# Kernel optimization log

Measured on AMD Instinct MI355X. Metric: run time of the kernel, lower is better.

## Reference

```python
import jax, jax.numpy as jnp
import numpy as np

B, T, D = 2, 2048, 1024
HEADS, UNITS = 16, 64
OUT_DIM = 1024
_LARGE_BIAS = 10000.0


def _uniform(key, shape, fan_in, fan_out):
    limit = np.sqrt(6.0 / (fan_in + fan_out))
    return jax.random.uniform(key, shape, jnp.float32, -limit, limit)


def setup_inputs() -> dict:
    key = jax.random.key(0)
    kx, kq, kk, kv, ko = jax.random.split(key, 5)
    x = jax.random.normal(kx, (B, T, D), jnp.float32)
    mask = jnp.ones((B, T), jnp.int32)
    Wq = _uniform(kq, (D, HEADS * UNITS), D, UNITS)
    Wk = _uniform(kk, (D, HEADS * UNITS), D, UNITS)
    Wv = _uniform(kv, (D, HEADS * UNITS), D, UNITS)
    Wo = _uniform(ko, (HEADS * UNITS, OUT_DIM), HEADS * UNITS, OUT_DIM)
    return {"x": x, "mask": mask, "Wq": Wq, "Wk": Wk, "Wv": Wv, "Wo": Wo}


def reference(x, mask, Wq, Wk, Wv, Wo):
    m = mask.astype(x.dtype)                      # [B, T]
    x = x * m[:, :, None]                         # zero padded positions
    b, t, _ = x.shape
    # projections, split heads: [B, T, H, U]
    q = (x @ Wq).reshape(b, t, HEADS, UNITS)
    k = (x @ Wk).reshape(b, t, HEADS, UNITS)
    v = (x @ Wv).reshape(b, t, HEADS, UNITS)
    # logits[b,h,i,j] = sum_u q[b,i,h,u] k[b,j,h,u]
    logits = jnp.einsum('bihu,bjhu->bhij', q, k) / np.sqrt(UNITS).astype(x.dtype)
    # causal (forward) mask: subtract large bias above the diagonal
    causal = jnp.triu(jnp.full((t, t), _LARGE_BIAS, x.dtype), k=1)
    logits = logits - causal
    # padding mask on key axis
    logits = logits - ((1.0 - m) * _LARGE_BIAS)[:, None, None, :]
    weights = jax.nn.softmax(logits, axis=-1)     # [B, H, T, T]
    attended = jnp.einsum('bhij,bjhu->bihu', weights, v)
    attended = attended.reshape(b, t, HEADS * UNITS)
    return attended @ Wo                          # [B, T, OUT_DIM]
```

## Files before the change

kernel.cpp:

```cpp
#include <hip/hip_runtime.h>
#include <stdint.h>
#include <stddef.h>

#define B_ 2
#define T_ 2048
#define D_ 1024
#define H_ 16
#define U_ 64
#define M_ (B_ * T_)
#define N_ (H_ * U_)

typedef __attribute__((ext_vector_type(4))) float f32x4;
typedef __attribute__((ext_vector_type(8))) short s16x8;
typedef __attribute__((ext_vector_type(8))) __bf16 b16x8;

static_assert(sizeof(s16x8) == 16, "frag size");

__device__ __forceinline__ unsigned short f2bf(float f) {
  unsigned int u = __float_as_uint(f);
  u += 0x7FFFu + ((u >> 16) & 1u);
  return (unsigned short)(u >> 16);
}

__device__ __forceinline__ float exp2_hw(float x) {
  float r;
  asm("v_exp_f32 %0, %1" : "=v"(r) : "v"(x));
  return r;
}
__device__ __forceinline__ unsigned int cvtpk_bf16(float lo, float hi) {
  unsigned int r;
  asm("v_cvt_pk_bf16_f32 %0, %1, %2" : "=v"(r) : "v"(lo), "v"(hi));
  return r;
}

template <typename V>
__device__ __forceinline__ auto mfma16_impl(V a, V b, f32x4 c, int)
    -> decltype(__builtin_amdgcn_mfma_f32_16x16x32_bf16(a, b, c, 0, 0, 0)) {
  return __builtin_amdgcn_mfma_f32_16x16x32_bf16(a, b, c, 0, 0, 0);
}
template <typename V>
__device__ __forceinline__ f32x4 mfma16_impl(V a, V b, f32x4 c, long) {
  return __builtin_amdgcn_mfma_f32_16x16x32_bf16(
      __builtin_bit_cast(b16x8, a), __builtin_bit_cast(b16x8, b), c, 0, 0, 0);
}
__device__ __forceinline__ f32x4 mfma16(s16x8 a, s16x8 b, f32x4 c) {
  return mfma16_impl(a, b, c, 0);
}

__device__ __forceinline__ void gld16(const unsigned short* g, unsigned short* l) {
  __builtin_amdgcn_global_load_lds(
      (const __attribute__((address_space(1))) void*)g,
      (__attribute__((address_space(3))) void*)l, 16, 0, 0);
}

__global__ void prep_kernel(const float* __restrict__ x, const int* __restrict__ mask,
                            const float* __restrict__ w0, const float* __restrict__ w1,
                            const float* __restrict__ w2, const float* __restrict__ w3,
                            unsigned short* __restrict__ o0, unsigned short* __restrict__ o1,
                            unsigned short* __restrict__ o2, unsigned short* __restrict__ o3,
                            unsigned short* __restrict__ xb) {
  const int tid = threadIdx.x;
  if (blockIdx.x < 1024) {
    __shared__ float tile[64][65];
    const int id = blockIdx.x;
    const int mz = id >> 8, by = (id >> 4) & 15, bx = id & 15;
    const float* w;
    unsigned short* o;
    switch (mz) {
      case 0: w = w0; o = o0; break;
      case 1: w = w1; o = o1; break;
      case 2: w = w2; o = o2; break;
      default: w = w3; o = o3; break;
    }
    const int kb = by * 64, nb = bx * 64;
    const int r0 = tid >> 6, c = tid & 63;
#pragma unroll
    for (int i = 0; i < 16; i++) {
      int r = i * 4 + r0;
      tile[r][c] = w[(size_t)(kb + r) * 1024 + nb + c];
    }
    __syncthreads();
#pragma unroll
    for (int i = 0; i < 16; i++) {
      int r = i * 4 + r0;
      o[(size_t)(nb + r) * 1024 + kb + c] = f2bf(tile[c][r]);
    }
  } else {
    const int idx = ((blockIdx.x - 1024) * 256 + tid) * 4;
    const int row = idx >> 10;
    const float m = (float)mask[row];
    float4 v = *(const float4*)(x + idx);
    ushort4 o;
    o.x = f2bf(v.x * m);
    o.y = f2bf(v.y * m);
    o.z = f2bf(v.z * m);
    o.w = f2bf(v.w * m);
    *(ushort4*)(xb + idx) = o;
  }
}

template <int MODE>
__device__ __forceinline__ void gemm64_body(const unsigned short* __restrict__ A,
                                            const unsigned short* __restrict__ Bt,
                                            void* __restrict__ Cout) {
  constexpr int Kd = 1024, Nd = 1024;
  __shared__ unsigned short la[128 * 64];
  __shared__ unsigned short lb[128 * 64];
  const int tid = threadIdx.x;
  const int lane = tid & 63;
  const int w = tid >> 6;
  const int mb = blockIdx.y * 128, nb = blockIdx.x * 128;
  const int wm = (w >> 1) * 64, wn = (w & 1) * 64;
  const int lr = lane & 15, lg = lane >> 4;
  const int srow = tid >> 3;
  const int scol = (tid & 7) * 8;
  const int sc = scol ^ ((srow & 7) << 3);
  const unsigned short* gA = A + (size_t)(mb + srow) * Kd + sc;
  const unsigned short* gB = Bt + (size_t)(nb + srow) * Kd + sc;
  unsigned short* lA = la + srow * 64 + scol;
  unsigned short* lB = lb + srow * 64 + scol;
  const int rsw = (lr & 7) << 3;

  f32x4 acc[4][4] = {};

  for (int kt = 0; kt < Kd; kt += 64) {
#pragma unroll
    for (int i = 0; i < 4; i++) {
      gld16(gA + kt + (size_t)(i * 32) * Kd, lA + i * 32 * 64);
      gld16(gB + kt + (size_t)(i * 32) * Kd, lB + i * 32 * 64);
    }
    __syncthreads();
#pragma unroll
    for (int ks = 0; ks < 2; ks++) {
      const int kc = (ks * 32 + lg * 8) ^ rsw;
      s16x8 af[4], bfr[4];
#pragma unroll
      for (int i = 0; i < 4; i++)
        af[i] = *(const s16x8*)(la + (wm + i * 16 + lr) * 64 + kc);
#pragma unroll
      for (int j = 0; j < 4; j++)
        bfr[j] = *(const s16x8*)(lb + (wn + j * 16 + lr) * 64 + kc);
#pragma unroll
      for (int i = 0; i < 4; i++)
#pragma unroll
        for (int j = 0; j < 4; j++)
          acc[i][j] = mfma16(af[i], bfr[j], acc[i][j]);
    }
    __syncthreads();
  }

#pragma unroll
  for (int i = 0; i < 4; i++)
#pragma unroll
    for (int j = 0; j < 4; j++) {
      const int col = nb + wn + j * 16 + lr;
      const int rowb = mb + wm + i * 16 + lg * 4;
      if (MODE == 1) {
        float* C = (float*)Cout;
#pragma unroll
        for (int r = 0; r < 4; r++) C[(size_t)(rowb + r) * Nd + col] = acc[i][j][r];
      } else if (MODE == 0) {
        unsigned short* C = (unsigned short*)Cout;
#pragma unroll
        for (int r = 0; r < 4; r++) C[(size_t)(rowb + r) * Nd + col] = f2bf(acc[i][j][r]);
      } else {
        unsigned short* C = (unsigned short*)Cout;
        const size_t vrow = ((size_t)(rowb >> 11) * 16 + (col >> 6)) * 64 + (col & 63);
        ushort4 o;
#pragma unroll
        for (int r = 0; r < 4; r++) ((unsigned short*)&o)[r] = f2bf(acc[i][j][r]);
        *(ushort4*)(C + vrow * T_ + (rowb & 2047)) = o;
      }
    }
}

__global__ __launch_bounds__(256) void gemm_qkv(const unsigned short* __restrict__ A,
                                                const unsigned short* __restrict__ wq,
                                                const unsigned short* __restrict__ wk,
                                                const unsigned short* __restrict__ wv,
                                                unsigned short* __restrict__ cq,
                                                unsigned short* __restrict__ ck,
                                                unsigned short* __restrict__ vt) {
  if (blockIdx.z == 0) {
    gemm64_body<0>(A, wq, cq);
  } else if (blockIdx.z == 1) {
    gemm64_body<0>(A, wk, ck);
  } else {
    gemm64_body<2>(A, wv, vt);
  }
}

__global__ __launch_bounds__(256) void gemm_out(const unsigned short* __restrict__ A,
                                                const unsigned short* __restrict__ woT,
                                                float* __restrict__ C) {
  gemm64_body<1>(A, woT, C);
}

__global__ __launch_bounds__(64) void attn17_kernel(const unsigned short* __restrict__ Q,
                                                    const unsigned short* __restrict__ K,
                                                    const unsigned short* __restrict__ Vt,
                                                    const int* __restrict__ mask,
                                                    unsigned short* __restrict__ att) {
  __shared__ unsigned short pbuf[32 * 64];
  const int lane = threadIdx.x & 63;
  const int li = lane & 15, lg = lane >> 4;
  const int bh = blockIdx.x & 31;
  const int b = bh >> 4, h = bh & 15;
  const int pr = blockIdx.x >> 5;

  const float CS = 0.125f * 1.44269504089f;
  const float PB = 10000.0f * 1.44269504089f;
  const float THR = 8.0f;

  const unsigned short* Kb = K + (size_t)(b * T_) * 1024 + h * 64;
  const unsigned short* Vtb = Vt + (size_t)bh * 64 * T_;
  const int* mk = mask + b * T_;

  const int xr = (li & 3) << 5;
  char* pbb = (char*)pbuf;

  for (int g = 0; g < 2; g++) {
    const int qg = g == 0 ? (63 - pr) : pr;
    const int q0 = qg * 32;

    s16x8 qf[2][2];
#pragma unroll
    for (int f = 0; f < 2; f++) {
      const unsigned short* qrow = Q + ((size_t)(b * T_) + q0 + f * 16 + li) * 1024 + h * 64;
      qf[f][0] = *(const s16x8*)(qrow + lg * 8);
      qf[f][1] = *(const s16x8*)(qrow + 32 + lg * 8);
    }

    const int iq0 = q0 + li, iq1 = q0 + 16 + li;

    float mrun[2] = {-1e30f, -1e30f};
    f32x4 lp[2] = {};
    f32x4 acc[4][2] = {};
    s16x8 vf[4][2];

    const int ntiles = (q0 + 95) >> 6;

    auto loadK = [&](s16x8 (&dst)[4][2], int jb) {
#pragma unroll
      for (int jf = 0; jf < 4; jf++) {
        const unsigned short* kr = Kb + (size_t)(jb + jf * 16 + li) * 1024 + lg * 8;
        dst[jf][0] = *(const s16x8*)kr;
        dst[jf][1] = *(const s16x8*)(kr + 32);
      }
    };
    auto loadM = [&](int4 (&dst)[4], int jb) {
#pragma unroll
      for (int jf = 0; jf < 4; jf++)
        dst[jf] = *(const int4*)(mk + jb + jf * 16 + lg * 4);
    };
    auto loadV = [&](int jb) {
#pragma unroll
      for (int uf = 0; uf < 4; uf++) {
        const unsigned short* vr = Vtb + (size_t)(uf * 16 + li) * T_ + jb + lg * 8;
        vf[uf][0] = *(const s16x8*)vr;
        vf[uf][1] = *(const s16x8*)(vr + 32);
      }
    };
    auto qk = [&](f32x4 (&s)[4][2], s16x8 (&kc)[4][2]) {
      __builtin_amdgcn_s_setprio(1);
#pragma unroll
      for (int jf = 0; jf < 4; jf++) {
        f32x4 z = {};
        s[jf][0] = mfma16(kc[jf][0], qf[0][0], z);
        s[jf][0] = mfma16(kc[jf][1], qf[0][1], s[jf][0]);
        f32x4 z2 = {};
        s[jf][1] = mfma16(kc[jf][0], qf[1][0], z2);
        s[jf][1] = mfma16(kc[jf][1], qf[1][1], s[jf][1]);
      }
      __builtin_amdgcn_s_setprio(0);
    };
    auto smw = [&](f32x4 (&s)[4][2], int4 (&mv)[4], int jb) {
      const bool diag = (jb + 64 > q0);
      const int band = (mv[0].x & mv[0].y & mv[0].z & mv[0].w) &
                       (mv[1].x & mv[1].y & mv[1].z & mv[1].w) &
                       (mv[2].x & mv[2].y & mv[2].z & mv[2].w) &
                       (mv[3].x & mv[3].y & mv[3].z & mv[3].w);
      const bool noBias = __all(band != 0);
#pragma unroll
      for (int f = 0; f < 2; f++) {
        const int iq = f ? iq1 : iq0;
        f32x4 pv4 = {-3e38f, -3e38f, -3e38f, -3e38f};
        if (noBias) {
#pragma unroll
          for (int jf = 0; jf < 4; jf++) {
            f32x4 zz = s[jf][f] * CS;
            if (diag) {
#pragma unroll
              for (int r = 0; r < 4; r++)
                if (jb + jf * 16 + lg * 4 + r > iq) zz[r] = -1e30f;
            }
            s[jf][f] = zz;
            pv4 = __builtin_elementwise_max(pv4, zz);
          }
        } else {
#pragma unroll
          for (int jf = 0; jf < 4; jf++) {
            f32x4 zz;
#pragma unroll
            for (int r = 0; r < 4; r++) {
              float z = fmaf(s[jf][f][r], CS, ((&mv[jf].x)[r] ? 0.f : -PB));
              if (diag && (jb + jf * 16 + lg * 4 + r > iq)) z = -1e30f;
              zz[r] = z;
            }
            s[jf][f] = zz;
            pv4 = __builtin_elementwise_max(pv4, zz);
          }
        }
        const float pmax = fmaxf(fmaxf(pv4[0], pv4[1]), fmaxf(pv4[2], pv4[3]));
        if (!__all(pmax <= mrun[f] + THR)) {
          float rmax = fmaxf(pmax, __shfl_xor(pmax, 16));
          rmax = fmaxf(rmax, __shfl_xor(rmax, 32));
          const float mnew = fmaxf(mrun[f], rmax);
          const float al = exp2_hw(mrun[f] - mnew);
          lp[f] *= al;
#pragma unroll
          for (int uf = 0; uf < 4; uf++) acc[uf][f] *= al;
          mrun[f] = mnew;
        }
        const float mm = mrun[f];
#pragma unroll
        for (int jf = 0; jf < 4; jf++) {
          f32x4 p;
#pragma unroll
          for (int r = 0; r < 4; r++) p[r] = exp2_hw(s[jf][f][r] - mm);
          lp[f] += p;
          uint2 w2;
          w2.x = cvtpk_bf16(p[0], p[1]);
          w2.y = cvtpk_bf16(p[2], p[3]);
          const int wb = (((f * 16 + li) * 64 + jf * 16 + lg * 4) * 2) ^ xr;
          *(uint2*)(pbb + wb) = w2;
        }
      }
    };
    auto pv = [&]() {
      s16x8 pfrag[2][2];
#pragma unroll
      for (int f = 0; f < 2; f++)
#pragma unroll
        for (int hh = 0; hh < 2; hh++) {
          const int rd = (((f * 16 + li) * 64 + hh * 32 + lg * 8) * 2) ^ xr;
          pfrag[f][hh] = *(const s16x8*)(pbb + rd);
        }
      __builtin_amdgcn_s_setprio(1);
#pragma unroll
      for (int uf = 0; uf < 4; uf++)
#pragma unroll
        for (int f = 0; f < 2; f++) {
          acc[uf][f] = mfma16(vf[uf][0], pfrag[f][0], acc[uf][f]);
          acc[uf][f] = mfma16(vf[uf][1], pfrag[f][1], acc[uf][f]);
        }
      __builtin_amdgcn_s_setprio(0);
    };

    s16x8 kA[4][2], kB[4][2];
    f32x4 sA[4][2], sB[4][2];
    int4 mA[4], mB[4];

    loadK(kA, 0);
    loadM(mA, 0);
    qk(sA, kA);
    if (ntiles > 1) {
      loadK(kB, 64);
      loadM(mB, 64);
    }

    int t = 0;
    while (true) {
      {
        const int jb = t * 64;
        loadV(jb);
        smw(sA, mA, jb);
        if (t + 1 < ntiles) qk(sB, kB);
        if (t + 2 < ntiles) {
          loadK(kA, (t + 2) * 64);
          loadM(mA, (t + 2) * 64);
        }
        pv();
      }
      if (t + 1 >= ntiles) break;
      {
        const int jb = (t + 1) * 64;
        loadV(jb);
        smw(sB, mB, jb);
        if (t + 2 < ntiles) qk(sA, kA);
        if (t + 3 < ntiles) {
          loadK(kB, (t + 3) * 64);
          loadM(mB, (t + 3) * 64);
        }
        pv();
      }
      t += 2;
      if (t >= ntiles) break;
    }

#pragma unroll
    for (int f = 0; f < 2; f++) {
      float l = (lp[f][0] + lp[f][1]) + (lp[f][2] + lp[f][3]);
      l += __shfl_xor(l, 16);
      l += __shfl_xor(l, 32);
      const float inv = 1.0f / l;
      unsigned short* arow = att + ((size_t)(b * T_) + q0 + f * 16 + li) * 1024 + h * 64;
#pragma unroll
      for (int uf = 0; uf < 4; uf++) {
        ushort4 o;
#pragma unroll
        for (int r = 0; r < 4; r++)
          ((unsigned short*)&o)[r] = __builtin_bit_cast(unsigned short, (__bf16)(acc[uf][f][r] * inv));
        *(ushort4*)(arow + uf * 16 + lg * 4) = o;
      }
    }
  }
}

extern "C" void kernel_launch(void* const* d_in, const int* in_sizes, int n_in,
                              void* d_out, int out_size, void* d_ws, size_t ws_size,
                              hipStream_t stream) {
  const float* x = (const float*)d_in[0];
  const int* mask = (const int*)d_in[1];
  const float* Wq = (const float*)d_in[2];
  const float* Wk = (const float*)d_in[3];
  const float* Wv = (const float*)d_in[4];
  const float* Wo = (const float*)d_in[5];

  const size_t MB = 1u << 20;
  char* ws = (char*)d_ws;
  unsigned short* wqT = (unsigned short*)(ws + 0 * MB);
  unsigned short* wkT = (unsigned short*)(ws + 2 * MB);
  unsigned short* wvT = (unsigned short*)(ws + 4 * MB);
  unsigned short* woT = (unsigned short*)(ws + 6 * MB);
  unsigned short* xb  = (unsigned short*)(ws + 8 * MB);
  unsigned short* qb  = (unsigned short*)(ws + 16 * MB);
  unsigned short* kb  = (unsigned short*)(ws + 24 * MB);
  unsigned short* vt  = (unsigned short*)(ws + 32 * MB);
  unsigned short* att = xb;
  (void)ws_size; (void)in_sizes; (void)n_in; (void)out_size;

  prep_kernel<<<dim3(5120), 256, 0, stream>>>(x, mask, Wq, Wk, Wv, Wo,
                                              wqT, wkT, wvT, woT, xb);
  gemm_qkv<<<dim3(8, 32, 3), 256, 0, stream>>>(xb, wqT, wkT, wvT, qb, kb, vt);
  attn17_kernel<<<dim3(1024), 64, 0, stream>>>(qb, kb, vt, mask, att);
  gemm_out<<<dim3(8, 32), 256, 0, stream>>>(att, woT, (float*)d_out);
}
```

Baseline: 140.9 us.

## Vectorize weight transpose and retile output GEMM to 128x64 blocks

The weight prep kernel now loads float4 rows into a padded shared tile and writes packed bf16 pairs as 16-byte stores, replacing scalar loads and 2-byte stores. The output projection gets its own 128x64-tile GEMM with 2x4 MFMA fragments per wave, which doubles the grid to 512 blocks for better CU occupancy on the 256-block problem. This trades per-block data reuse for more parallelism. The change also assumes a cvtpk_bf16 helper already exists.

```diff
diff --git a/kernel.cpp b/kernel.cpp
--- a/kernel.cpp
+++ b/kernel.cpp
@@ -61,7 +61,7 @@
                             unsigned short* __restrict__ xb) {
   const int tid = threadIdx.x;
   if (blockIdx.x < 1024) {
-    __shared__ float tile[64][65];
+    __shared__ float tile[64][68];
     const int id = blockIdx.x;
     const int mz = id >> 8, by = (id >> 4) & 15, bx = id & 15;
     const float* w;
@@ -73,17 +73,23 @@
       default: w = w3; o = o3; break;
     }
     const int kb = by * 64, nb = bx * 64;
-    const int r0 = tid >> 6, c = tid & 63;
-#pragma unroll
-    for (int i = 0; i < 16; i++) {
-      int r = i * 4 + r0;
-      tile[r][c] = w[(size_t)(kb + r) * 1024 + nb + c];
-    }
+    const int r = tid >> 4, c4 = (tid & 15) * 4;
+#pragma unroll
+    for (int i = 0; i < 4; i++)
+      *(float4*)&tile[r + i * 16][c4] =
+          *(const float4*)(w + (size_t)(kb + r + i * 16) * 1024 + nb + c4);
     __syncthreads();
 #pragma unroll
-    for (int i = 0; i < 16; i++) {
-      int r = i * 4 + r0;
-      o[(size_t)(nb + r) * 1024 + kb + c] = f2bf(tile[c][r]);
+    for (int i = 0; i < 2; i++) {
+      const int idx = tid + i * 256;
+      const int n = idx >> 3;
+      const int k0 = (idx & 7) * 8;
+      unsigned int u0 = cvtpk_bf16(tile[k0 + 0][n], tile[k0 + 1][n]);
+      unsigned int u1 = cvtpk_bf16(tile[k0 + 2][n], tile[k0 + 3][n]);
+      unsigned int u2 = cvtpk_bf16(tile[k0 + 4][n], tile[k0 + 5][n]);
+      unsigned int u3 = cvtpk_bf16(tile[k0 + 6][n], tile[k0 + 7][n]);
+      uint4 o4 = {u0, u1, u2, u3};
+      *(uint4*)(o + (size_t)(nb + n) * 1024 + kb + k0) = o4;
     }
   } else {
     const int idx = ((blockIdx.x - 1024) * 256 + tid) * 4;
@@ -155,11 +161,7 @@
     for (int j = 0; j < 4; j++) {
       const int col = nb + wn + j * 16 + lr;
       const int rowb = mb + wm + i * 16 + lg * 4;
-      if (MODE == 1) {
-        float* C = (float*)Cout;
-#pragma unroll
-        for (int r = 0; r < 4; r++) C[(size_t)(rowb + r) * Nd + col] = acc[i][j][r];
-      } else if (MODE == 0) {
+      if (MODE == 0) {
         unsigned short* C = (unsigned short*)Cout;
 #pragma unroll
         for (int r = 0; r < 4; r++) C[(size_t)(rowb + r) * Nd + col] = f2bf(acc[i][j][r]);
@@ -193,7 +195,62 @@
 __global__ __launch_bounds__(256) void gemm_out(const unsigned short* __restrict__ A,
                                                 const unsigned short* __restrict__ woT,
                                                 float* __restrict__ C) {
-  gemm64_body<1>(A, woT, C);
+  constexpr int Kd = 1024, Nd = 1024;
+  __shared__ unsigned short la[128 * 64];
+  __shared__ unsigned short lb[64 * 64];
+  const int tid = threadIdx.x;
+  const int lane = tid & 63;
+  const int w = tid >> 6;
+  const int mb = blockIdx.y * 128, nb = blockIdx.x * 64;
+  const int wm = w * 32;
+  const int lr = lane & 15, lg = lane >> 4;
+  const int srow = tid >> 3;
+  const int scol = (tid & 7) * 8;
+  const int sc = scol ^ ((srow & 7) << 3);
+  const unsigned short* gA = A + (size_t)(mb + srow) * Kd + sc;
+  const unsigned short* gB = woT + (size_t)(nb + srow) * Kd + sc;
+  unsigned short* lA = la + srow * 64 + scol;
+  unsigned short* lB = lb + srow * 64 + scol;
+  const int rsw = (lr & 7) << 3;
+
+  f32x4 acc[2][4] = {};
+
+  for (int kt = 0; kt < Kd; kt += 64) {
+#pragma unroll
+    for (int i = 0; i < 4; i++)
+      gld16(gA + kt + (size_t)(i * 32) * Kd, lA + i * 32 * 64);
+#pragma unroll
+    for (int i = 0; i < 2; i++)
+      gld16(gB + kt + (size_t)(i * 32) * Kd, lB + i * 32 * 64);
+    __syncthreads();
+#pragma unroll
+    for (int ks = 0; ks < 2; ks++) {
+      const int kc = (ks * 32 + lg * 8) ^ rsw;
+      s16x8 af[2], bfr[4];
+#pragma unroll
+      for (int i = 0; i < 2; i++)
+        af[i] = *(const s16x8*)(la + (wm + i * 16 + lr) * 64 + kc);
+#pragma unroll
+      for (int j = 0; j < 4; j++)
+        bfr[j] = *(const s16x8*)(lb + (j * 16 + lr) * 64 + kc);
+#pragma unroll
+      for (int i = 0; i < 2; i++)
+#pragma unroll
+        for (int j = 0; j < 4; j++)
+          acc[i][j] = mfma16(af[i], bfr[j], acc[i][j]);
+    }
+    __syncthreads();
+  }
+
+#pragma unroll
+  for (int i = 0; i < 2; i++)
+#pragma unroll
+    for (int j = 0; j < 4; j++) {
+      const int col = nb + j * 16 + lr;
+      const int rowb = mb + wm + i * 16 + lg * 4;
+#pragma unroll
+      for (int r = 0; r < 4; r++) C[(size_t)(rowb + r) * Nd + col] = acc[i][j][r];
+    }
 }
 
 __global__ __launch_bounds__(64) void attn17_kernel(const unsigned short* __restrict__ Q,
@@ -444,5 +501,5 @@
                                               wqT, wkT, wvT, woT, xb);
   gemm_qkv<<<dim3(8, 32, 3), 256, 0, stream>>>(xb, wqT, wkT, wvT, qb, kb, vt);
   attn17_kernel<<<dim3(1024), 64, 0, stream>>>(qb, kb, vt, mask, att);
-  gemm_out<<<dim3(8, 32), 256, 0, stream>>>(att, woT, (float*)d_out);
-}
+  gemm_out<<<dim3(16, 32), 256, 0, stream>>>(att, woT, (float*)d_out);
+}
```

Result: faster. 137.3 us (median of 3 runs) (-2.5%).
